# Kernel tuning notes

Measured on AMD Instinct MI355X. Metric: run time of the kernel, lower is better.

## Reference

```python
import jax, jax.numpy as jnp
import numpy as np

N_NODES = 100000
N_EDGES = 800000
EDGE_NAMES = ["ei_connected_to", "ei_ordered_next", "ei_represents", "ei_represented_by",
              "ei_neighboring_vertical", "ei_neighboring_horizontal", "ei_contains",
              "ei_order", "ei_perpendicular"]
AGGRS_L2 = ["sum", "sum", "mean", "mean", "sum", "sum", "mean"]


def _glorot(key, shape):
    fan_in, fan_out = shape[-2], shape[-1]
    s = (2.0 / (fan_in + fan_out)) ** 0.5
    return jax.random.normal(key, shape, dtype=jnp.float32) * s


def setup_inputs() -> dict:
    key = jax.random.key(0)
    ks = iter(jax.random.split(key, 32))
    inp = {"x": jax.random.normal(next(ks), (N_NODES, 6), dtype=jnp.float32)}
    for name in EDGE_NAMES:
        inp[name] = jax.random.randint(next(ks), (2, N_EDGES), 0, N_NODES, dtype=jnp.int32)
    inp.update(
        W0n=_glorot(next(ks), (2, 6, 16)), W0r=_glorot(next(ks), (2, 6, 16)),
        b0=jnp.zeros((2, 16), jnp.float32),
        W1n=_glorot(next(ks), (2, 16, 32)), W1r=_glorot(next(ks), (2, 16, 32)),
        b1=jnp.zeros((2, 32), jnp.float32),
        P1=_glorot(next(ks), (16, 32)), pb1=jnp.zeros((32,), jnp.float32),
        W2n=_glorot(next(ks), (7, 32, 64)), W2r=_glorot(next(ks), (7, 32, 64)),
        b2=jnp.zeros((7, 64), jnp.float32),
        P2=_glorot(next(ks), (32, 64)), pb2=jnp.zeros((64,), jnp.float32),
    )
    return inp


def _hetero_conv(x, edges, aggrs, Wn, Wr, b):
    # Per-relation GraphConv: out_d = aggr(x[src]->dst) @ Wn_r + x @ Wr_r + b_r,
    # summed across relations (HeteroConv aggr='sum'). Loop is over a small fixed
    # set of relation types (structurally distinct), not data dims.
    n = x.shape[0]
    out = jnp.zeros((n, Wn.shape[-1]), x.dtype)
    for i, (ei, aggr) in enumerate(zip(edges, aggrs)):
        src, dst = ei[0], ei[1]
        msg = jax.ops.segment_sum(x[src], dst, num_segments=n)  # scatter-add gather
        if aggr == "mean":
            cnt = jax.ops.segment_sum(jnp.ones_like(dst, dtype=x.dtype), dst, num_segments=n)
            msg = msg / jnp.maximum(cnt, 1.0)[:, None]
        out = out + msg @ Wn[i] + x @ Wr[i] + b[i]
    return out


def reference(x, W0n, W0r, b0, W1n, W1r, b1, P1, pb1, W2n, W2r, b2, P2, pb2,
              ei_connected_to, ei_ordered_next, ei_represents, ei_represented_by,
              ei_neighboring_vertical, ei_neighboring_horizontal, ei_contains,
              ei_order, ei_perpendicular):
    e01 = [ei_connected_to, ei_ordered_next]
    e2 = [ei_represents, ei_represented_by, ei_neighboring_vertical,
          ei_neighboring_horizontal, ei_contains, ei_order, ei_perpendicular]
    # local head: 6 -> 16 (two sum relations)
    h = _hetero_conv(x, e01, ["sum", "sum"], W0n, W0r, b0)
    # residual block 1: 16 -> 32 (same two sum relations, linear residual projection)
    h = jax.nn.relu(_hetero_conv(h, e01, ["sum", "sum"], W1n, W1r, b1) + h @ P1 + pb1)
    # residual block 2: 32 -> 64 (seven relations, sum/mean aggregation)
    h = jax.nn.relu(_hetero_conv(h, e2, AGGRS_L2, W2n, W2r, b2) + h @ P2 + pb2)
    # final elementwise relu from SemanticModule.forward
    return jax.nn.relu(h)
```

## Files before the change

kernel.cpp:

```cpp
#include <hip/hip_runtime.h>

#define NN 100000
#define NE 800000
#define NRG 128
#define SPAN 784
#define CAP 8192
#define NBIN (9 * NRG)

typedef _Float16 f16;
typedef __attribute__((ext_vector_type(4))) _Float16 f16x4;
typedef __attribute__((ext_vector_type(8))) _Float16 f16x8;
typedef __attribute__((ext_vector_type(4))) float f32x4;
typedef __attribute__((ext_vector_type(2))) float f32x2;

struct EPtrs { const int* s[9]; const int* d[9]; };

__global__ __launch_bounds__(256) void prep_weights(
    const float* __restrict__ W0n, const float* __restrict__ W0r, const float* __restrict__ b0,
    const float* __restrict__ W1n, const float* __restrict__ W1r, const float* __restrict__ b1,
    const float* __restrict__ P1,  const float* __restrict__ pb1,
    const float* __restrict__ W2n, const float* __restrict__ W2r, const float* __restrict__ b2,
    const float* __restrict__ P2,  const float* __restrict__ pb2,
    float* __restrict__ wc0, float* __restrict__ bc0,
    float* __restrict__ wc1, float* __restrict__ bc1,
    f16*   __restrict__ b2frag, float* __restrict__ bc2,
    int*   __restrict__ cursor)
{
    int tid = threadIdx.x;
    for (int t = tid; t < NBIN; t += 256) cursor[t] = 0;

    for (int t = tid; t < 18 * 16; t += 256) {
        int row = t >> 4, col = t & 15;
        float v;
        if (row < 6)       v = W0n[row * 16 + col];
        else if (row < 12) v = W0n[96 + (row - 6) * 16 + col];
        else               v = W0r[(row - 12) * 16 + col] + W0r[96 + (row - 12) * 16 + col];
        wc0[t] = v;
    }
    for (int t = tid; t < 16; t += 256) bc0[t] = b0[t] + b0[16 + t];

    for (int t = tid; t < 48 * 32; t += 256) {
        int row = t >> 5, col = t & 31;
        float v;
        if (row < 16)      v = W1n[row * 32 + col];
        else if (row < 32) v = W1n[512 + (row - 16) * 32 + col];
        else { int rr = row - 32; v = W1r[rr * 32 + col] + W1r[512 + rr * 32 + col] + P1[rr * 32 + col]; }
        wc1[t] = v;
    }
    for (int t = tid; t < 32; t += 256) bc1[t] = b1[t] + b1[32 + t] + pb1[t];

    for (int t = tid; t < 256 * 64; t += 256) {
        int j = t & 7, lane = (t >> 3) & 63, ntk = t >> 9;
        int nt = ntk & 3, kt = ntk >> 2;
        int k = kt * 32 + (lane >> 4) * 8 + j;
        int n = nt * 16 + (lane & 15);
        float v;
        if (k < 224) v = W2n[k * 64 + n];
        else {
            int rr = k - 224;
            v = P2[rr * 64 + n];
            #pragma unroll
            for (int r = 0; r < 7; ++r) v += W2r[r * 2048 + rr * 64 + n];
        }
        b2frag[t] = (f16)v;
    }
    for (int t = tid; t < 64; t += 256) {
        float v = pb2[t];
        #pragma unroll
        for (int r = 0; r < 7; ++r) v += b2[r * 64 + t];
        bc2[t] = v;
    }
}

__global__ __launch_bounds__(256) void passA(EPtrs ep, int* __restrict__ cursor,
                                             unsigned* __restrict__ binbuf)
{
    int r = blockIdx.y;
    int e0 = blockIdx.x * 4096;
    int tid = threadIdx.x;
    __shared__ int h[NRG];
    __shared__ int gb[NRG];

    if (tid < NRG) h[tid] = 0;
    __syncthreads();

    const int* dp = ep.d[r];
    const int* sp = ep.s[r];
    unsigned wv[16];
    int rgk[16];
    int lrk[16];
    #pragma unroll
    for (int k = 0; k < 16; ++k) {
        int e = e0 + k * 256 + tid;
        rgk[k] = -1;
        if (e < NE) {
            int d = dp[e];
            int sv = sp[e];
            int g = d / SPAN;
            int l = d - g * SPAN;
            wv[k] = ((unsigned)l << 17) | (unsigned)sv;
            rgk[k] = g;
            lrk[k] = atomicAdd(&h[g], 1);
        }
    }
    __syncthreads();
    if (tid < NRG) {
        int v = h[tid];
        gb[tid] = (v > 0) ? atomicAdd(&cursor[r * NRG + tid], v) : 0;
    }
    __syncthreads();
    #pragma unroll
    for (int k = 0; k < 16; ++k) {
        if (rgk[k] >= 0) {
            int p = gb[rgk[k]] + lrk[k];
            if (p < CAP)
                binbuf[((size_t)(r * NRG + rgk[k])) * CAP + p] = wv[k];
        }
    }
}

__global__ __launch_bounds__(256) void passB(const unsigned* __restrict__ binbuf,
                                             const int* __restrict__ cursor,
                                             int* __restrict__ deg, int* __restrict__ off,
                                             int* __restrict__ eidx)
{
    int bin = blockIdx.x;
    int r = bin >> 7, rg = bin & (NRG - 1);
    int lo = rg * SPAN;
    int n_here = min(SPAN, NN - lo);
    int tid = threadIdx.x;
    __shared__ int h[SPAN];
    __shared__ int wsum[4];

    int sz = min(cursor[bin], CAP);
    const unsigned* bp = binbuf + (size_t)bin * CAP;

    for (int i = tid; i < SPAN; i += 256) h[i] = 0;
    __syncthreads();

    unsigned wv[32];
    int rk[32];
    #pragma unroll
    for (int k = 0; k < 32; ++k) {
        int e = tid + k * 256;
        if (e < sz) {
            unsigned w = bp[e];
            wv[k] = w;
            rk[k] = atomicAdd(&h[w >> 17], 1);
        }
    }
    __syncthreads();

    int i0 = tid * 4;
    int dstash[4];
    int s = 0;
    #pragma unroll
    for (int k = 0; k < 4; ++k) {
        int i = i0 + k;
        int v = (i < SPAN) ? h[i] : 0;
        dstash[k] = v;
        s += v;
    }
    int lane = tid & 63, wid = tid >> 6;
    int incl = s;
    #pragma unroll
    for (int ofs = 1; ofs < 64; ofs <<= 1) {
        int u = __shfl_up(incl, ofs, 64);
        if (lane >= ofs) incl += u;
    }
    if (lane == 63) wsum[wid] = incl;
    __syncthreads();
    if (tid == 0) {
        int a = wsum[0], b = wsum[1], c = wsum[2];
        wsum[0] = 0; wsum[1] = a; wsum[2] = a + b; wsum[3] = a + b + c;
    }
    __syncthreads();
    int run = incl - s + wsum[wid];
    int base = bin * CAP;
    #pragma unroll
    for (int k = 0; k < 4; ++k) {
        int i = i0 + k;
        if (i < SPAN) {
            int v = dstash[k];
            h[i] = run;
            if (i < n_here) {
                deg[r * NN + lo + i] = v;
                off[r * NN + lo + i] = base + run + v;
            }
            run += v;
        }
    }
    __syncthreads();

    #pragma unroll
    for (int k = 0; k < 32; ++k) {
        int e = tid + k * 256;
        if (e < sz) {
            unsigned w = wv[k];
            eidx[base + h[w >> 17] + rk[k]] = (int)(w & 0x1FFFF);
        }
    }
}

__global__ __launch_bounds__(256) void t0f(const float* __restrict__ x,
                                           const int* __restrict__ deg, const int* __restrict__ off,
                                           const int* __restrict__ eidx,
                                           const float* __restrict__ wc0, const float* __restrict__ bc0,
                                           f16* __restrict__ h0h)
{
    __shared__ float sw[288 + 16];
    for (int t = threadIdx.x; t < 304; t += 256) sw[t] = (t < 288) ? wc0[t] : bc0[t - 288];
    __syncthreads();
    int t = blockIdx.x * 256 + threadIdx.x;
    int node = t >> 2;
    if (node >= NN) return;
    int l = t & 3;
    int r = l >> 1, p = l & 1;

    float m[6] = {0, 0, 0, 0, 0, 0};
    {
        int e1 = off[r * NN + node];
        int e0 = e1 - deg[r * NN + node];
        int e = e0 + p;
        for (; e + 2 < e1; e += 4) {
            int sA = eidx[e], sB = eidx[e + 2];
            const float2* pA = reinterpret_cast<const float2*>(x + (size_t)sA * 6);
            const float2* pB = reinterpret_cast<const float2*>(x + (size_t)sB * 6);
            float2 a0 = pA[0], a1 = pA[1], a2 = pA[2];
            float2 b0 = pB[0], b1 = pB[1], b2 = pB[2];
            m[0] += a0.x + b0.x; m[1] += a0.y + b0.y;
            m[2] += a1.x + b1.x; m[3] += a1.y + b1.y;
            m[4] += a2.x + b2.x; m[5] += a2.y + b2.y;
        }
        if (e < e1) {
            int sA = eidx[e];
            const float2* pA = reinterpret_cast<const float2*>(x + (size_t)sA * 6);
            float2 a0 = pA[0], a1 = pA[1], a2 = pA[2];
            m[0] += a0.x; m[1] += a0.y; m[2] += a1.x; m[3] += a1.y; m[4] += a2.x; m[5] += a2.y;
        }
    }
    float mo[6];
    #pragma unroll
    for (int k = 0; k < 6; ++k) {
        m[k] += __shfl_xor(m[k], 1, 64);
        mo[k] = __shfl_xor(m[k], 2, 64);
    }
    int baseOwn = r * 96, baseOth = (1 - r) * 96;
    float xv[6];
    {
        const float2* xp = reinterpret_cast<const float2*>(x + (size_t)node * 6);
        float2 a = xp[0], b = xp[1], c = xp[2];
        xv[0] = a.x; xv[1] = a.y; xv[2] = b.x; xv[3] = b.y; xv[4] = c.x; xv[5] = c.y;
    }
    int dc = l * 4;
    float acc[4];
    #pragma unroll
    for (int j = 0; j < 4; ++j) acc[j] = sw[288 + dc + j];
    #pragma unroll
    for (int k = 0; k < 6; ++k) {
        #pragma unroll
        for (int j = 0; j < 4; ++j) {
            acc[j] = fmaf(m[k],  sw[baseOwn + k * 16 + dc + j], acc[j]);
            acc[j] = fmaf(mo[k], sw[baseOth + k * 16 + dc + j], acc[j]);
            acc[j] = fmaf(xv[k], sw[192 + k * 16 + dc + j], acc[j]);
        }
    }
    f16x4 o;
    #pragma unroll
    for (int j = 0; j < 4; ++j) o[j] = (f16)acc[j];
    *reinterpret_cast<f16x4*>(h0h + (size_t)node * 16 + dc) = o;
}

__global__ __launch_bounds__(256) void g1t(const int* __restrict__ deg, const int* __restrict__ off,
                                           const int* __restrict__ eidx, const f16* __restrict__ h0h,
                                           const float* __restrict__ wc1, const float* __restrict__ bc1,
                                           f16* __restrict__ h1h, unsigned* __restrict__ h1q)
{
    __shared__ float sw[1536 + 32];
    __shared__ float ms[64][33];
    for (int t = threadIdx.x; t < 1568; t += 256) sw[t] = (t < 1536) ? wc1[t] : bc1[t - 1536];

    int tid = threadIdx.x;
    int nloc = tid >> 2, l = tid & 3;
    int node = blockIdx.x * 64 + nloc;

    if (node < NN) {
        #pragma unroll 1
        for (int r = 0; r < 2; ++r) {
            int e1 = off[r * NN + node];
            int e0 = e1 - deg[r * NN + node];
            float a0 = 0.f, a1 = 0.f, a2 = 0.f, a3 = 0.f;
            int e = e0;
            for (; e + 4 <= e1; e += 4) {
                int sA = eidx[e], sB = eidx[e + 1], sC = eidx[e + 2], sD = eidx[e + 3];
                f16x4 vA = *reinterpret_cast<const f16x4*>(h0h + (size_t)sA * 16 + l * 4);
                f16x4 vB = *reinterpret_cast<const f16x4*>(h0h + (size_t)sB * 16 + l * 4);
                f16x4 vC = *reinterpret_cast<const f16x4*>(h0h + (size_t)sC * 16 + l * 4);
                f16x4 vD = *reinterpret_cast<const f16x4*>(h0h + (size_t)sD * 16 + l * 4);
                a0 += (float)vA[0] + (float)vB[0] + (float)vC[0] + (float)vD[0];
                a1 += (float)vA[1] + (float)vB[1] + (float)vC[1] + (float)vD[1];
                a2 += (float)vA[2] + (float)vB[2] + (float)vC[2] + (float)vD[2];
                a3 += (float)vA[3] + (float)vB[3] + (float)vC[3] + (float)vD[3];
            }
            for (; e < e1; ++e) {
                f16x4 v = *reinterpret_cast<const f16x4*>(h0h + (size_t)eidx[e] * 16 + l * 4);
                a0 += (float)v[0]; a1 += (float)v[1]; a2 += (float)v[2]; a3 += (float)v[3];
            }
            ms[nloc][r * 16 + l * 4 + 0] = a0;
            ms[nloc][r * 16 + l * 4 + 1] = a1;
            ms[nloc][r * 16 + l * 4 + 2] = a2;
            ms[nloc][r * 16 + l * 4 + 3] = a3;
        }
    }
    __syncthreads();
    if (node >= NN) return;

    int c0 = l * 8;
    float acc[8];
    #pragma unroll
    for (int j = 0; j < 8; ++j) acc[j] = sw[1536 + c0 + j];
    #pragma unroll
    for (int k = 0; k < 32; ++k) {
        float s = ms[nloc][k];
        #pragma unroll
        for (int j = 0; j < 8; ++j) acc[j] = fmaf(s, sw[k * 32 + c0 + j], acc[j]);
    }
    {
        const f16x8* hp = reinterpret_cast<const f16x8*>(h0h + (size_t)node * 16);
        f16x8 a = hp[0], b = hp[1];
        #pragma unroll
        for (int k = 0; k < 8; ++k) {
            float s0 = (float)a[k], s1 = (float)b[k];
            #pragma unroll
            for (int j = 0; j < 8; ++j)
                acc[j] = fmaf(s0, sw[(32 + k) * 32 + c0 + j], fmaf(s1, sw[(40 + k) * 32 + c0 + j], acc[j]));
        }
    }
    #pragma unroll
    for (int j = 0; j < 8; ++j) acc[j] = fmaxf(acc[j], 0.f);

    f16x8 o;
    #pragma unroll
    for (int j = 0; j < 8; ++j) o[j] = (f16)acc[j];
    *reinterpret_cast<f16x8*>(h1h + (size_t)node * 32 + c0) = o;

    int w0 = __builtin_amdgcn_cvt_pk_fp8_f32(acc[0], acc[1], 0, false);
    w0 = __builtin_amdgcn_cvt_pk_fp8_f32(acc[2], acc[3], w0, true);
    int w1 = __builtin_amdgcn_cvt_pk_fp8_f32(acc[4], acc[5], 0, false);
    w1 = __builtin_amdgcn_cvt_pk_fp8_f32(acc[6], acc[7], w1, true);
    *reinterpret_cast<uint2*>(h1q + (size_t)node * 8 + l * 2) = make_uint2((unsigned)w0, (unsigned)w1);
}

__global__ __launch_bounds__(256, 8) void g2t2(const int* __restrict__ deg, const int* __restrict__ off,
                                               const int* __restrict__ eidx, const unsigned* __restrict__ h1q,
                                               const f16* __restrict__ h1h, const f16* __restrict__ b2frag,
                                               const float* __restrict__ bc2, float* __restrict__ out)
{
    __shared__ f16 cat[16][264];

    int tid = threadIdx.x;
    int nloc = tid >> 4;
    int lane16 = tid & 15;
    int node = blockIdx.x * 16 + nloc;

    if (lane16 >= 14) {
        int part = lane16 - 14;
        const f16x8* hp = reinterpret_cast<const f16x8*>(h1h + (size_t)node * 32 + part * 16);
        f16x8 v0 = hp[0], v1 = hp[1];
        *reinterpret_cast<f16x8*>(&cat[nloc][224 + part * 16]) = v0;
        *reinterpret_cast<f16x8*>(&cat[nloc][224 + part * 16 + 8]) = v1;
    } else {
        int r = lane16 >> 1;
        int half = lane16 & 1;
        int d = deg[(r + 2) * NN + node];
        int e1 = off[(r + 2) * NN + node];
        int e0 = e1 - d;

        f32x2 acc[8];
        #pragma unroll
        for (int q = 0; q < 8; ++q) acc[q] = (f32x2){0.f, 0.f};

        const uint4* tbl = reinterpret_cast<const uint4*>(h1q);
        int e = e0;
        for (; e + 2 <= e1; e += 2) {
            int sA = eidx[e], sB = eidx[e + 1];
            uint4 qA = tbl[(size_t)sA * 2 + half];
            uint4 qB = tbl[(size_t)sB * 2 + half];
            acc[0] += __builtin_amdgcn_cvt_pk_f32_fp8(qA.x, false);
            acc[1] += __builtin_amdgcn_cvt_pk_f32_fp8(qA.x, true);
            acc[2] += __builtin_amdgcn_cvt_pk_f32_fp8(qA.y, false);
            acc[3] += __builtin_amdgcn_cvt_pk_f32_fp8(qA.y, true);
            acc[4] += __builtin_amdgcn_cvt_pk_f32_fp8(qA.z, false);
            acc[5] += __builtin_amdgcn_cvt_pk_f32_fp8(qA.z, true);
            acc[6] += __builtin_amdgcn_cvt_pk_f32_fp8(qA.w, false);
            acc[7] += __builtin_amdgcn_cvt_pk_f32_fp8(qA.w, true);
            acc[0] += __builtin_amdgcn_cvt_pk_f32_fp8(qB.x, false);
            acc[1] += __builtin_amdgcn_cvt_pk_f32_fp8(qB.x, true);
            acc[2] += __builtin_amdgcn_cvt_pk_f32_fp8(qB.y, false);
            acc[3] += __builtin_amdgcn_cvt_pk_f32_fp8(qB.y, true);
            acc[4] += __builtin_amdgcn_cvt_pk_f32_fp8(qB.z, false);
            acc[5] += __builtin_amdgcn_cvt_pk_f32_fp8(qB.z, true);
            acc[6] += __builtin_amdgcn_cvt_pk_f32_fp8(qB.w, false);
            acc[7] += __builtin_amdgcn_cvt_pk_f32_fp8(qB.w, true);
        }
        if (e < e1) {
            int sA = eidx[e];
            uint4 qA = tbl[(size_t)sA * 2 + half];
            acc[0] += __builtin_amdgcn_cvt_pk_f32_fp8(qA.x, false);
            acc[1] += __builtin_amdgcn_cvt_pk_f32_fp8(qA.x, true);
            acc[2] += __builtin_amdgcn_cvt_pk_f32_fp8(qA.y, false);
            acc[3] += __builtin_amdgcn_cvt_pk_f32_fp8(qA.y, true);
            acc[4] += __builtin_amdgcn_cvt_pk_f32_fp8(qA.z, false);
            acc[5] += __builtin_amdgcn_cvt_pk_f32_fp8(qA.z, true);
            acc[6] += __builtin_amdgcn_cvt_pk_f32_fp8(qA.w, false);
            acc[7] += __builtin_amdgcn_cvt_pk_f32_fp8(qA.w, true);
        }

        float sc = (r == 2 || r == 3 || r == 6) ? (1.0f / (float)max(d, 1)) : 1.0f;
        f16x8 o0, o1;
        #pragma unroll
        for (int q = 0; q < 4; ++q) {
            o0[q * 2 + 0] = (f16)(acc[q][0] * sc);
            o0[q * 2 + 1] = (f16)(acc[q][1] * sc);
            o1[q * 2 + 0] = (f16)(acc[4 + q][0] * sc);
            o1[q * 2 + 1] = (f16)(acc[4 + q][1] * sc);
        }
        *reinterpret_cast<f16x8*>(&cat[nloc][r * 32 + half * 16]) = o0;
        *reinterpret_cast<f16x8*>(&cat[nloc][r * 32 + half * 16 + 8]) = o1;
    }

    int lane = tid & 63, w = tid >> 6;
    int quad = lane >> 4, col0 = lane & 15;
    float bcv = bc2[w * 16 + col0];

    f16x8 bfr[8];
    #pragma unroll
    for (int kt = 0; kt < 8; ++kt)
        bfr[kt] = *reinterpret_cast<const f16x8*>(b2frag + ((size_t)(kt * 4 + w) * 64 + lane) * 8);

    __syncthreads();

    f32x4 acc = (f32x4){0.f, 0.f, 0.f, 0.f};
    #pragma unroll
    for (int kt = 0; kt < 8; ++kt) {
        f16x8 a = *reinterpret_cast<const f16x8*>(&cat[col0][kt * 32 + quad * 8]);
        acc = __builtin_amdgcn_mfma_f32_16x16x32_f16(a, bfr[kt], acc, 0, 0, 0);
    }

    int row0 = blockIdx.x * 16 + quad * 4;
    #pragma unroll
    for (int i = 0; i < 4; ++i)
        out[(size_t)(row0 + i) * 64 + w * 16 + col0] = fmaxf(acc[i] + bcv, 0.f);
}

extern "C" void kernel_launch(void* const* d_in, const int* in_sizes, int n_in,
                              void* d_out, int out_size, void* d_ws, size_t ws_size,
                              hipStream_t stream)
{
    const float* x = (const float*)d_in[0];
    EPtrs ep;
    for (int i = 0; i < 9; ++i) { const int* p = (const int*)d_in[1 + i]; ep.s[i] = p; ep.d[i] = p + NE; }
    const float* W0n = (const float*)d_in[10]; const float* W0r = (const float*)d_in[11];
    const float* b0  = (const float*)d_in[12];
    const float* W1n = (const float*)d_in[13]; const float* W1r = (const float*)d_in[14];
    const float* b1  = (const float*)d_in[15];
    const float* P1  = (const float*)d_in[16]; const float* pb1 = (const float*)d_in[17];
    const float* W2n = (const float*)d_in[18]; const float* W2r = (const float*)d_in[19];
    const float* b2  = (const float*)d_in[20];
    const float* P2  = (const float*)d_in[21]; const float* pb2 = (const float*)d_in[22];
    float* out = (float*)d_out;
    char* ws = (char*)d_ws;

    size_t off_b = 0;
    auto alloc = [&](size_t b) { size_t o = off_b; off_b += (b + 255) & ~(size_t)255; return o; };
    size_t o_wc0 = alloc(288 * 4);   size_t o_bc0 = alloc(16 * 4);
    size_t o_wc1 = alloc(1536 * 4);  size_t o_bc1 = alloc(32 * 4);
    size_t o_b2f = alloc(16384 * 2); size_t o_bc2 = alloc(64 * 4);
    size_t o_h0h = alloc((size_t)NN * 16 * 2);
    size_t o_h1q = alloc((size_t)NN * 32);
    size_t o_h1h = alloc((size_t)NN * 32 * 2);
    size_t o_bin = alloc((size_t)NBIN * CAP * 4);
    size_t o_deg = alloc((size_t)9 * NN * 4);
    size_t o_off = alloc((size_t)9 * NN * 4);
    size_t o_eid = alloc((size_t)NBIN * CAP * 4);
    size_t o_cur = alloc((size_t)NBIN * 4);
    (void)ws_size;

    float* wc0 = (float*)(ws + o_wc0); float* bc0 = (float*)(ws + o_bc0);
    float* wc1 = (float*)(ws + o_wc1); float* bc1 = (float*)(ws + o_bc1);
    f16*   b2f = (f16*)(ws + o_b2f);   float* bc2 = (float*)(ws + o_bc2);
    f16*   h0h = (f16*)(ws + o_h0h);
    unsigned* h1q = (unsigned*)(ws + o_h1q);
    f16*   h1h = (f16*)(ws + o_h1h);
    unsigned* binbuf = (unsigned*)(ws + o_bin);
    int*   deg = (int*)(ws + o_deg);
    int*   offp = (int*)(ws + o_off);
    int*   eid = (int*)(ws + o_eid);
    int*   cur = (int*)(ws + o_cur);

    dim3 B(256);
    prep_weights<<<1, B, 0, stream>>>(W0n, W0r, b0, W1n, W1r, b1, P1, pb1,
                                      W2n, W2r, b2, P2, pb2,
                                      wc0, bc0, wc1, bc1, b2f, bc2, cur);
    passA<<<dim3((NE + 4095) / 4096, 9), B, 0, stream>>>(ep, cur, binbuf);
    passB<<<NBIN, B, 0, stream>>>(binbuf, cur, deg, offp, eid);

    t0f<<<(NN * 4 + 255) / 256, B, 0, stream>>>(x, deg, offp, eid, wc0, bc0, h0h);
    g1t<<<(NN + 63) / 64, B, 0, stream>>>(deg, offp, eid, h0h, wc1, bc1, h1h, h1q);
    g2t2<<<NN / 16, B, 0, stream>>>(deg, offp, eid, h1q, h1h, b2f, bc2, out);
}
```

Measured before the change: 334.9 us.

## Stage bucketed edge writes in shared memory for coalesced global stores

```diff
diff --git a/kernel.cpp b/kernel.cpp
--- a/kernel.cpp
+++ b/kernel.cpp
@@ -77,9 +77,14 @@
 {
     int r = blockIdx.y;
     int e0 = blockIdx.x * 4096;
+    int cnt = min(4096, NE - e0);
     int tid = threadIdx.x;
     __shared__ int h[NRG];
+    __shared__ int bs[NRG + 1];
+    __shared__ int cl[NRG];
     __shared__ int gb[NRG];
+    __shared__ int auxtot;
+    __shared__ unsigned pk[4096];
 
     if (tid < NRG) h[tid] = 0;
     __syncthreads();
@@ -88,7 +93,6 @@
     const int* sp = ep.s[r];
     unsigned wv[16];
     int rgk[16];
-    int lrk[16];
     #pragma unroll
     for (int k = 0; k < 16; ++k) {
         int e = e0 + k * 256 + tid;
@@ -100,22 +104,52 @@
             int l = d - g * SPAN;
             wv[k] = ((unsigned)l << 17) | (unsigned)sv;
             rgk[k] = g;
-            lrk[k] = atomicAdd(&h[g], 1);
-        }
-    }
-    __syncthreads();
+            atomicAdd(&h[g], 1);
+        }
+    }
+    __syncthreads();
+
+    int vcnt = 0, incl = 0;
     if (tid < NRG) {
-        int v = h[tid];
-        gb[tid] = (v > 0) ? atomicAdd(&cursor[r * NRG + tid], v) : 0;
-    }
-    __syncthreads();
+        vcnt = h[tid];
+        incl = vcnt;
+        int lane = tid & 63;
+        #pragma unroll
+        for (int ofs = 1; ofs < 64; ofs <<= 1) {
+            int u = __shfl_up(incl, ofs, 64);
+            if (lane >= ofs) incl += u;
+        }
+        if (tid == 63) auxtot = incl;
+    }
+    __syncthreads();
+    if (tid < NRG) {
+        int excl = incl - vcnt + ((tid >= 64) ? auxtot : 0);
+        bs[tid] = excl;
+        cl[tid] = excl;
+        gb[tid] = (vcnt > 0) ? atomicAdd(&cursor[r * NRG + tid], vcnt) : 0;
+        if (tid == NRG - 1) bs[NRG] = excl + vcnt;
+    }
+    __syncthreads();
+
     #pragma unroll
     for (int k = 0; k < 16; ++k) {
         if (rgk[k] >= 0) {
-            int p = gb[rgk[k]] + lrk[k];
-            if (p < CAP)
-                binbuf[((size_t)(r * NRG + rgk[k])) * CAP + p] = wv[k];
-        }
+            int p = atomicAdd(&cl[rgk[k]], 1);
+            pk[p] = wv[k];
+        }
+    }
+    __syncthreads();
+
+    for (int i = tid; i < cnt; i += 256) {
+        int loB = 0, hiB = NRG;
+        while (hiB - loB > 1) {
+            int mid = (loB + hiB) >> 1;
+            if (bs[mid] <= i) loB = mid; else hiB = mid;
+        }
+        int b = loB;
+        int pos = gb[b] + (i - bs[b]);
+        if (pos < CAP)
+            binbuf[((size_t)(r * NRG + b)) * CAP + pos] = pk[i];
     }
 }
 
@@ -131,6 +165,7 @@
     int tid = threadIdx.x;
     __shared__ int h[SPAN];
     __shared__ int wsum[4];
+    __shared__ int stage[CAP];
 
     int sz = min(cursor[bin], CAP);
     const unsigned* bp = binbuf + (size_t)bin * CAP;
@@ -197,9 +232,11 @@
         int e = tid + k * 256;
         if (e < sz) {
             unsigned w = wv[k];
-            eidx[base + h[w >> 17] + rk[k]] = (int)(w & 0x1FFFF);
-        }
-    }
+            stage[h[w >> 17] + rk[k]] = (int)(w & 0x1FFFF);
+        }
+    }
+    __syncthreads();
+    for (int i = tid; i < sz; i += 256) eidx[base + i] = stage[i];
 }
 
 __global__ __launch_bounds__(256) void t0f(const float* __restrict__ x,
```

Result: faster. 310.8 us (-7.2%).
